# Kernel tuning notes

Measured on AMD Instinct MI355X. Metric: run time of the kernel, lower is better.

## Reference

```python
import jax, jax.numpy as jnp
import numpy as np
import math

NUM_HEADS = 16
THETA = 10000.0


def _rope(x, token_pos, theta):
    # x: [B, H, S, d_k]; token_pos: [S]
    d_k = x.shape[-1]
    freqs = 1.0 / theta ** (jnp.arange(0, d_k, 2, dtype=jnp.float32) / d_k)  # [d_k/2]
    angles = token_pos.astype(jnp.float32)[:, None] * freqs[None, :]         # [S, d_k/2]
    cos, sin = jnp.cos(angles), jnp.sin(angles)
    x1 = x[..., 0::2]
    x2 = x[..., 1::2]
    out1 = x1 * cos - x2 * sin
    out2 = x1 * sin + x2 * cos
    # interleave back: (..., d_k/2, 2) -> (..., d_k)
    return jnp.stack([out1, out2], axis=-1).reshape(x.shape)


def setup_inputs() -> dict:
    key = jax.random.key(0)
    ks = jax.random.split(key, 5)
    B, S, D = 4, 2048, 1024
    scale = 0.02
    return {
        "x": jax.random.normal(ks[0], (B, S, D), dtype=jnp.float32),
        "token_pos": jnp.arange(S, dtype=jnp.int64 if jax.config.jax_enable_x64 else jnp.int32),
        "Wq": jax.random.normal(ks[1], (D, D), dtype=jnp.float32) * scale,
        "Wk": jax.random.normal(ks[2], (D, D), dtype=jnp.float32) * scale,
        "Wv": jax.random.normal(ks[3], (D, D), dtype=jnp.float32) * scale,
        "Wo": jax.random.normal(ks[4], (D, D), dtype=jnp.float32) * scale,
    }


def reference(x, token_pos, Wq, Wk, Wv, Wo):
    B, S, D = x.shape
    H = NUM_HEADS
    d_k = D // H
    # projections (Linear without bias: y = x @ W^T, W is [out, in])
    def proj(W):
        y = jnp.einsum('bsd,ed->bse', x, W)
        return y.reshape(B, S, H, d_k).transpose(0, 2, 1, 3)  # [B,H,S,d_k]
    q, k, v = proj(Wq), proj(Wk), proj(Wv)
    q = _rope(q, token_pos, THETA)
    k = _rope(k, token_pos, THETA)
    scores = jnp.einsum('bhqd,bhkd->bhqk', q, k) / math.sqrt(d_k)
    causal = jnp.tril(jnp.ones((S, S), dtype=bool))
    scores = jnp.where(causal, scores, -jnp.inf)
    attn = jax.nn.softmax(scores, axis=-1)
    out = jnp.einsum('bhqk,bhkd->bhqd', attn, v)            # [B,H,S,d_k]
    out = out.transpose(0, 2, 1, 3).reshape(B, S, D)
    return jnp.einsum('bsd,ed->bse', out, Wo)
```

## Files before the change

### kernel.cpp

```cpp
#include <hip/hip_runtime.h>

typedef unsigned short u16;
typedef __bf16 bf16x8 __attribute__((ext_vector_type(8)));
typedef float f32x4 __attribute__((ext_vector_type(4)));
typedef u16 u16x8 __attribute__((ext_vector_type(8)));

#define B_ 4
#define S_ 2048
#define D_ 1024
#define H_ 16
#define LOG2E 1.44269504f

__device__ inline u16 f2bf(float f) {
  unsigned u = __float_as_uint(f);
  u = u + 0x7fffu + ((u >> 16) & 1u);
  return (u16)(u >> 16);
}
__device__ inline u16 f2bf_hw(float f) {
  __bf16 b = (__bf16)f;
  return __builtin_bit_cast(u16, b);
}
__device__ inline float bf2f(u16 h) {
  return __uint_as_float(((unsigned)h) << 16);
}
__device__ inline void gload_lds16(const u16* g, u16* l) {
  __builtin_amdgcn_global_load_lds((const __attribute__((address_space(1))) void*)g,
                                   (__attribute__((address_space(3))) void*)l, 16, 0, 0);
}
__device__ inline float fast_exp2(float x) {
  float r;
  asm("v_exp_f32 %0, %1" : "=v"(r) : "v"(x));
  return r;
}

__global__ __launch_bounds__(256) void k_f32_to_bf16(const float* __restrict__ src,
                                                     u16* __restrict__ dst, int n4) {
  int i = blockIdx.x * 256 + threadIdx.x;
  if (i >= n4) return;
  float4 v = reinterpret_cast<const float4*>(src)[i];
  ushort4 o;
  o.x = f2bf(v.x); o.y = f2bf(v.y); o.z = f2bf(v.z); o.w = f2bf(v.w);
  reinterpret_cast<ushort4*>(dst)[i] = o;
}

__global__ __launch_bounds__(256) void k_cvt_w4(const float* __restrict__ w0,
                                                const float* __restrict__ w1,
                                                const float* __restrict__ w2,
                                                const float* __restrict__ w3,
                                                u16* __restrict__ dst) {
  int i = blockIdx.x * 256 + threadIdx.x;
  const int tensor = i >> 18;
  const int local = i & 262143;
  const float* s = tensor == 0 ? w0 : tensor == 1 ? w1 : tensor == 2 ? w2 : w3;
  float4 v = reinterpret_cast<const float4*>(s)[local];
  ushort4 o;
  o.x = f2bf(v.x); o.y = f2bf(v.y); o.z = f2bf(v.z); o.w = f2bf(v.w);
  reinterpret_cast<ushort4*>(dst + (size_t)tensor * 1048576)[local] = o;
}

__global__ __launch_bounds__(256) void k_rope_table(const int* __restrict__ pos,
                                                    float2* __restrict__ tab) {
  int idx = blockIdx.x * 256 + threadIdx.x;
  if (idx >= S_ * 32) return;
  int s = idx >> 5, i = idx & 31;
  float freq = powf(10000.0f, -(float)i * (1.0f / 32.0f));
  float ang = (float)pos[s] * freq;
  float sn, c;
  sincosf(ang, &sn, &c);
  tab[idx] = make_float2(c, sn);
}

__global__ __launch_bounds__(256) void k_rope_k(u16* __restrict__ kb,
                                                const float2* __restrict__ tab) {
  int idx = blockIdx.x * 256 + threadIdx.x;
  const int row = idx >> 7;
  const int s = row & 2047;
  const int chunk = idx & 127;
  u16* p = kb + ((size_t)row << 10) + chunk * 8;
  u16x8 v = *reinterpret_cast<u16x8*>(p);
  const float4* tp = reinterpret_cast<const float4*>(tab + s * 32 + (chunk & 7) * 4);
  float4 t0 = tp[0], t1 = tp[1];
  float cc[4] = {t0.x, t0.z, t1.x, t1.z};
  float ss[4] = {t0.y, t0.w, t1.y, t1.w};
  u16x8 o;
#pragma unroll
  for (int u = 0; u < 4; u++) {
    float x1 = bf2f(v[2 * u]), x2 = bf2f(v[2 * u + 1]);
    o[2 * u]     = f2bf(x1 * cc[u] - x2 * ss[u]);
    o[2 * u + 1] = f2bf(x1 * ss[u] + x2 * cc[u]);
  }
  *reinterpret_cast<u16x8*>(p) = o;
}

__global__ __launch_bounds__(256) void k_gemm_qkv(const u16* __restrict__ A,
                                                  const u16* __restrict__ Bcat,
                                                  u16* __restrict__ Ccat,
                                                  u16* __restrict__ Vt) {
  __shared__ u16 As[128 * 64];
  __shared__ u16 Bs[128 * 64];
  const int K = 1024;
  const int swz = (blockIdx.x & 7) * 192 + (blockIdx.x >> 3);
  const int bx = swz % 24;
  const int by = swz / 24;
  const int m0 = by << 7, n0 = bx << 7;
  const int tid = threadIdx.x;
  const int lane = tid & 63;
  const int wv = tid >> 6;
  const int wm = (wv >> 1) << 6;
  const int wn = (wv & 1) << 6;
  const int r = lane & 15, g = lane >> 4;

  f32x4 acc[4][4] = {};

  const int srow0 = tid >> 3;
  const int scol = (((tid & 7) ^ ((tid >> 3) & 7)) * 8);
  const int csw = r & 7;

  for (int k0 = 0; k0 < K; k0 += 64) {
#pragma unroll
    for (int i = 0; i < 4; i++)
      gload_lds16(A + (size_t)(m0 + srow0 + 32 * i) * K + k0 + scol,
                  As + tid * 8 + i * 2048);
#pragma unroll
    for (int i = 0; i < 4; i++)
      gload_lds16(Bcat + (size_t)(n0 + srow0 + 32 * i) * K + k0 + scol,
                  Bs + tid * 8 + i * 2048);
    __syncthreads();
#pragma unroll
    for (int ks = 0; ks < 2; ks++) {
      bf16x8 af[4], bfr[4];
#pragma unroll
      for (int i = 0; i < 4; i++)
        af[i] = *reinterpret_cast<const bf16x8*>(
            &As[(wm + i * 16 + r) * 64 + (((ks * 4 + g) ^ csw) * 8)]);
#pragma unroll
      for (int t = 0; t < 4; t++)
        bfr[t] = *reinterpret_cast<const bf16x8*>(
            &Bs[(wn + t * 16 + r) * 64 + (((ks * 4 + g) ^ csw) * 8)]);
#pragma unroll
      for (int i = 0; i < 4; i++)
#pragma unroll
        for (int t = 0; t < 4; t++)
          acc[i][t] = __builtin_amdgcn_mfma_f32_16x16x32_bf16(af[i], bfr[t], acc[i][t], 0, 0, 0);
    }
    __syncthreads();
  }

  const int bq = n0 >> 10;
  const int c0 = n0 & 1023;
  if (bq == 2) {
#pragma unroll
    for (int i = 0; i < 4; i++) {
#pragma unroll
      for (int t = 0; t < 4; t++) {
        const int row = m0 + wm + i * 16 + g * 4;
        const int col = c0 + wn + t * 16 + r;
        const int b = row >> 11, s0 = row & 2047;
        const int h = col >> 6, d = col & 63;
        ushort4 o;
        o.x = f2bf(acc[i][t][0]); o.y = f2bf(acc[i][t][1]);
        o.z = f2bf(acc[i][t][2]); o.w = f2bf(acc[i][t][3]);
        *reinterpret_cast<ushort4*>(
            Vt + (((size_t)(b * 16 + h) * 64 + d) << 11) + s0) = o;
      }
    }
  } else {
    u16* Cb = Ccat + (size_t)bq * (8192 * 1024);
#pragma unroll
    for (int i = 0; i < 4; i++) {
#pragma unroll
      for (int t = 0; t < 4; t++) {
        const int row = m0 + wm + i * 16 + g * 4;
        const int col = c0 + wn + t * 16 + r;
#pragma unroll
        for (int j = 0; j < 4; j++)
          Cb[(size_t)(row + j) * 1024 + col] = f2bf(acc[i][t][j]);
      }
    }
  }
}

__global__ __launch_bounds__(256) void k_gemm_bt(const u16* __restrict__ A,
                                                 const u16* __restrict__ Bw,
                                                 float* __restrict__ C,
                                                 int M, int N, int K) {
  __shared__ u16 As[128 * 64];
  __shared__ u16 Bs[128 * 64];
  const int nbx = N >> 7;
  const int swz = (blockIdx.x & 7) * (gridDim.x >> 3) + (blockIdx.x >> 3);
  const int bx = swz % nbx;
  const int by = swz / nbx;
  const int m0 = by << 7, n0 = bx << 7;
  const int tid = threadIdx.x;
  const int lane = tid & 63;
  const int wv = tid >> 6;
  const int wm = (wv >> 1) << 6;
  const int wn = (wv & 1) << 6;
  const int r = lane & 15, g = lane >> 4;

  f32x4 acc[4][4] = {};

  const int srow0 = tid >> 3;
  const int scol = (((tid & 7) ^ ((tid >> 3) & 7)) * 8);
  const int csw = r & 7;

  for (int k0 = 0; k0 < K; k0 += 64) {
#pragma unroll
    for (int i = 0; i < 4; i++)
      gload_lds16(A + (size_t)(m0 + srow0 + 32 * i) * K + k0 + scol,
                  As + tid * 8 + i * 2048);
#pragma unroll
    for (int i = 0; i < 4; i++)
      gload_lds16(Bw + (size_t)(n0 + srow0 + 32 * i) * K + k0 + scol,
                  Bs + tid * 8 + i * 2048);
    __syncthreads();
#pragma unroll
    for (int ks = 0; ks < 2; ks++) {
      bf16x8 af[4], bfr[4];
#pragma unroll
      for (int i = 0; i < 4; i++)
        af[i] = *reinterpret_cast<const bf16x8*>(
            &As[(wm + i * 16 + r) * 64 + (((ks * 4 + g) ^ csw) * 8)]);
#pragma unroll
      for (int t = 0; t < 4; t++)
        bfr[t] = *reinterpret_cast<const bf16x8*>(
            &Bs[(wn + t * 16 + r) * 64 + (((ks * 4 + g) ^ csw) * 8)]);
#pragma unroll
      for (int i = 0; i < 4; i++)
#pragma unroll
        for (int t = 0; t < 4; t++)
          acc[i][t] = __builtin_amdgcn_mfma_f32_16x16x32_bf16(af[i], bfr[t], acc[i][t], 0, 0, 0);
    }
    __syncthreads();
  }

#pragma unroll
  for (int i = 0; i < 4; i++) {
#pragma unroll
    for (int t = 0; t < 4; t++) {
      const int row = m0 + wm + i * 16 + g * 4;
      const int col = n0 + wn + t * 16 + r;
#pragma unroll
      for (int j = 0; j < 4; j++)
        C[(size_t)(row + j) * N + col] = acc[i][t][j];
    }
  }
}

__global__ __launch_bounds__(256) void k_attn14(const u16* __restrict__ Q,
                                                const u16* __restrict__ Kb,
                                                const u16* __restrict__ Vt,
                                                const float2* __restrict__ tab,
                                                u16* __restrict__ O) {
  __shared__ u16 Ks[64 * 64];
  __shared__ u16 Vs[64 * 64];
  __shared__ u16 Ps[4][32 * 64];

  const int bh = (blockIdx.x & 7) * 8 + ((blockIdx.x >> 3) & 7);
  const int qt = 15 - (blockIdx.x >> 6);
  const int b = bh >> 4, h = bh & 15;
  const int tid = threadIdx.x;
  const int lane = tid & 63, w = tid >> 6;
  const int g = lane >> 4, r = lane & 15;

  const u16* Kbase = Kb + (size_t)(b * S_) * 1024 + h * 64;
  const u16* Vbase = Vt + (size_t)bh * 64 * 2048;

  const int srow = tid >> 3;
  const int scol = ((tid & 7) * 8) ^ ((srow & 7) * 8);
  const int rsw = (r & 7) * 8;

  const int qbase = qt << 7;
  const int qrow0 = qbase + (w << 5);

  const float QSC = 0.125f * LOG2E;
  bf16x8 qf[2][2];
#pragma unroll
  for (int f = 0; f < 2; f++) {
    const int s = qrow0 + f * 16 + r;
    const u16* qrow = Q + (size_t)(b * S_ + s) * 1024 + h * 64;
    qf[f][0] = *reinterpret_cast<const bf16x8*>(qrow + g * 8);
    qf[f][1] = *reinterpret_cast<const bf16x8*>(qrow + 32 + g * 8);
    const float4* tp = reinterpret_cast<const float4*>(tab + s * 32);
#pragma unroll
    for (int c = 0; c < 2; c++) {
      float4 t0 = tp[c * 8 + g * 2], t1 = tp[c * 8 + g * 2 + 1];
      float cc[4] = {t0.x, t0.z, t1.x, t1.z};
      float ss[4] = {t0.y, t0.w, t1.y, t1.w};
      bf16x8 q = qf[f][c];
#pragma unroll
      for (int u = 0; u < 4; u++) {
        float x1 = (float)q[2 * u], x2 = (float)q[2 * u + 1];
        q[2 * u]     = (__bf16)((x1 * cc[u] - x2 * ss[u]) * QSC);
        q[2 * u + 1] = (__bf16)((x1 * ss[u] + x2 * cc[u]) * QSC);
      }
      qf[f][c] = q;
    }
  }

  bf16x8 ones;
#pragma unroll
  for (int u = 0; u < 8; u++) ones[u] = (__bf16)1.0f;

  f32x4 o_acc[2][4] = {};
  f32x4 lacc[2] = {};
  u16* pb0 = &Ps[w][r * 64];
  u16* pb1 = &Ps[w][(16 + r) * 64];

  const u16* kp0 = Kbase + (size_t)srow * 1024 + scol;
  const u16* kp1 = kp0 + 32 * 1024;
  const u16* vp0 = Vbase + (size_t)srow * 2048 + scol;
  const u16* vp1 = vp0 + 32 * 2048;

  const int kend = qbase + 128;
  for (int k0 = 0; k0 < kend; k0 += 64) {
    gload_lds16(kp0, Ks + tid * 8);
    gload_lds16(kp1, Ks + tid * 8 + 2048);
    gload_lds16(vp0, Vs + tid * 8);
    gload_lds16(vp1, Vs + tid * 8 + 2048);
    kp0 += 64 * 1024; kp1 += 64 * 1024; vp0 += 64; vp1 += 64;
    __syncthreads();

    if (k0 <= qrow0 + 31) {
      const int rem0 = qrow0 + 15 - k0;
      const int rem1 = qrow0 + 31 - k0;
      const int ktlim0 = rem0 < 0 ? 0 : (rem0 >= 48 ? 4 : (rem0 >> 4) + 1);
      const int ktlim1 = rem1 >= 48 ? 4 : (rem1 >> 4) + 1;
      const bool mask0 = (k0 + 63 > qrow0);
      const bool mask1 = (k0 + 63 > qrow0 + 16);

#pragma unroll
      for (int kt = 0; kt < 4; kt++) {
        const int pc = (kt * 16 + g * 4) ^ rsw;
        if (kt >= ktlim1) {
          ushort4 z = {0, 0, 0, 0};
          *reinterpret_cast<ushort4*>(pb0 + pc) = z;
          *reinterpret_cast<ushort4*>(pb1 + pc) = z;
          continue;
        }
        const int krow = kt * 16 + r;
        bf16x8 kf0 = *reinterpret_cast<const bf16x8*>(&Ks[krow * 64 + ((g * 8) ^ rsw)]);
        bf16x8 kf1 = *reinterpret_cast<const bf16x8*>(&Ks[krow * 64 + ((32 + g * 8) ^ rsw)]);
        f32x4 s0 = {}, s1 = {};
        if (kt < ktlim0) {
          s0 = __builtin_amdgcn_mfma_f32_16x16x32_bf16(kf0, qf[0][0], s0, 0, 0, 0);
          s0 = __builtin_amdgcn_mfma_f32_16x16x32_bf16(kf1, qf[0][1], s0, 0, 0, 0);
        }
        s1 = __builtin_amdgcn_mfma_f32_16x16x32_bf16(kf0, qf[1][0], s1, 0, 0, 0);
        s1 = __builtin_amdgcn_mfma_f32_16x16x32_bf16(kf1, qf[1][1], s1, 0, 0, 0);

        const int colb = k0 + kt * 16 + g * 4;
        float p0[4], p1[4];
        if (kt < ktlim0) {
          if (mask0) {
#pragma unroll
            for (int j = 0; j < 4; j++)
              if (colb + j > qrow0 + r) s0[j] = -1e30f;
          }
#pragma unroll
          for (int j = 0; j < 4; j++) p0[j] = fast_exp2(s0[j]);
        } else {
#pragma unroll
          for (int j = 0; j < 4; j++) p0[j] = 0.f;
        }
        if (mask1) {
#pragma unroll
          for (int j = 0; j < 4; j++)
            if (colb + j > qrow0 + 16 + r) s1[j] = -1e30f;
        }
#pragma unroll
        for (int j = 0; j < 4; j++) p1[j] = fast_exp2(s1[j]);

        ushort4 w0, w1;
        w0.x = f2bf_hw(p0[0]); w0.y = f2bf_hw(p0[1]); w0.z = f2bf_hw(p0[2]); w0.w = f2bf_hw(p0[3]);
        w1.x = f2bf_hw(p1[0]); w1.y = f2bf_hw(p1[1]); w1.z = f2bf_hw(p1[2]); w1.w = f2bf_hw(p1[3]);
        *reinterpret_cast<ushort4*>(pb0 + pc) = w0;
        *reinterpret_cast<ushort4*>(pb1 + pc) = w1;
      }
      asm volatile("s_waitcnt lgkmcnt(0)" ::: "memory");

#pragma unroll
      for (int kc = 0; kc < 2; kc++) {
        const int cb = (kc * 32 + g * 8) ^ rsw;
        bf16x8 pf0 = *reinterpret_cast<const bf16x8*>(pb0 + cb);
        bf16x8 pf1 = *reinterpret_cast<const bf16x8*>(pb1 + cb);
        lacc[0] = __builtin_amdgcn_mfma_f32_16x16x32_bf16(pf0, ones, lacc[0], 0, 0, 0);
        lacc[1] = __builtin_amdgcn_mfma_f32_16x16x32_bf16(pf1, ones, lacc[1], 0, 0, 0);
#pragma unroll
        for (int dt = 0; dt < 4; dt++) {
          bf16x8 vf = *reinterpret_cast<const bf16x8*>(
              &Vs[(dt * 16 + r) * 64 + ((kc * 32 + g * 8) ^ rsw)]);
          o_acc[0][dt] = __builtin_amdgcn_mfma_f32_16x16x32_bf16(pf0, vf, o_acc[0][dt], 0, 0, 0);
          o_acc[1][dt] = __builtin_amdgcn_mfma_f32_16x16x32_bf16(pf1, vf, o_acc[1][dt], 0, 0, 0);
        }
      }
    }
    __syncthreads();
  }

#pragma unroll
  for (int f = 0; f < 2; f++) {
    u16* orow = O + (size_t)(b * S_ + qrow0 + f * 16) * 1024 + h * 64;
#pragma unroll
    for (int j = 0; j < 4; j++) {
      const float rln = 1.0f / lacc[f][j];
#pragma unroll
      for (int dt = 0; dt < 4; dt++)
        orow[(size_t)(g * 4 + j) * 1024 + dt * 16 + r] = f2bf(o_acc[f][dt][j] * rln);
    }
  }
}

extern "C" void kernel_launch(void* const* d_in, const int* in_sizes, int n_in,
                              void* d_out, int out_size, void* d_ws, size_t ws_size,
                              hipStream_t stream) {
  const float* x  = (const float*)d_in[0];
  const int*   pos = (const int*)d_in[1];
  const float* Wq = (const float*)d_in[2];
  const float* Wk = (const float*)d_in[3];
  const float* Wv = (const float*)d_in[4];
  const float* Wo = (const float*)d_in[5];
  float* out = (float*)d_out;

  char* ws = (char*)d_ws;
  size_t off = 0;
  auto alloc = [&](size_t bytes) {
    void* p = ws + off;
    off += (bytes + 255) & ~(size_t)255;
    return p;
  };
  const size_t XB = (size_t)8192 * 1024 * 2;
  u16* xb  = (u16*)alloc(XB);
  u16* wqb = (u16*)alloc((size_t)1024 * 1024 * 2);
  u16* wkb = (u16*)alloc((size_t)1024 * 1024 * 2);
  u16* wvb = (u16*)alloc((size_t)1024 * 1024 * 2);
  u16* wob = (u16*)alloc((size_t)1024 * 1024 * 2);
  u16* qb  = (u16*)alloc(XB);
  u16* kb  = (u16*)alloc(XB);
  u16* ob  = (u16*)alloc(XB);
  u16* vt  = (u16*)alloc(XB);
  float2* tab = (float2*)alloc((size_t)2048 * 32 * sizeof(float2));
  (void)wkb; (void)wvb;

  k_f32_to_bf16<<<8192, 256, 0, stream>>>(x, xb, 2097152);
  k_cvt_w4<<<4096, 256, 0, stream>>>(Wq, Wk, Wv, Wo, wqb);
  k_rope_table<<<256, 256, 0, stream>>>(pos, tab);

  k_gemm_qkv<<<1536, 256, 0, stream>>>(xb, wqb, qb, vt);

  k_rope_k<<<4096, 256, 0, stream>>>(kb, tab);

  k_attn14<<<1024, 256, 0, stream>>>(qb, kb, vt, tab, ob);

  k_gemm_bt<<<512, 256, 0, stream>>>(ob, wob, out, 8192, 1024, 1024);
}
```

Before: 183.0 us.

## Double-buffer LDS tiles in QKV and output projection GEMMs

Both projection GEMM kernels now keep two LDS buffers per operand and issue the global-to-LDS loads for the next K tile before computing on the current one. Explicit vmcnt waits and raw s_barrier calls replace the old load, sync, compute, sync sequence. The aim is to hide global-load latency behind the MFMA work. LDS use per block doubles to 64 KB, which may lower occupancy, and correctness now depends on the hand-set vmcnt counts.

```diff
diff --git a/kernel.cpp b/kernel.cpp
--- a/kernel.cpp
+++ b/kernel.cpp
@@ -96,8 +96,8 @@
                                                   const u16* __restrict__ Bcat,
                                                   u16* __restrict__ Ccat,
                                                   u16* __restrict__ Vt) {
-  __shared__ u16 As[128 * 64];
-  __shared__ u16 Bs[128 * 64];
+  __shared__ u16 As[2][128 * 64];
+  __shared__ u16 Bs[2][128 * 64];
   const int K = 1024;
   const int swz = (blockIdx.x & 7) * 192 + (blockIdx.x >> 3);
   const int bx = swz % 24;
@@ -116,35 +116,56 @@
   const int scol = (((tid & 7) ^ ((tid >> 3) & 7)) * 8);
   const int csw = r & 7;
 
-  for (int k0 = 0; k0 < K; k0 += 64) {
-#pragma unroll
-    for (int i = 0; i < 4; i++)
-      gload_lds16(A + (size_t)(m0 + srow0 + 32 * i) * K + k0 + scol,
-                  As + tid * 8 + i * 2048);
-#pragma unroll
-    for (int i = 0; i < 4; i++)
-      gload_lds16(Bcat + (size_t)(n0 + srow0 + 32 * i) * K + k0 + scol,
-                  Bs + tid * 8 + i * 2048);
-    __syncthreads();
+  const u16* Ab = A + (size_t)(m0 + srow0) * K + scol;
+  const u16* Bb = Bcat + (size_t)(n0 + srow0) * K + scol;
+
+#define STAGEQ(k0v, bf) do {                                       \
+    const u16* a_ = Ab + (k0v);                                    \
+    const u16* b_ = Bb + (k0v);                                    \
+    gload_lds16(a_,                &As[bf][0] + tid * 8);          \
+    gload_lds16(a_ + (size_t)32 * K, &As[bf][0] + tid * 8 + 2048); \
+    gload_lds16(a_ + (size_t)64 * K, &As[bf][0] + tid * 8 + 4096); \
+    gload_lds16(a_ + (size_t)96 * K, &As[bf][0] + tid * 8 + 6144); \
+    gload_lds16(b_,                &Bs[bf][0] + tid * 8);          \
+    gload_lds16(b_ + (size_t)32 * K, &Bs[bf][0] + tid * 8 + 2048); \
+    gload_lds16(b_ + (size_t)64 * K, &Bs[bf][0] + tid * 8 + 4096); \
+    gload_lds16(b_ + (size_t)96 * K, &Bs[bf][0] + tid * 8 + 6144); \
+  } while (0)
+
+  STAGEQ(0, 0);
+
+  for (int t = 0; t < 16; ++t) {
+    const int bsel = t & 1;
+    if (t < 15) {
+      STAGEQ((t + 1) * 64, bsel ^ 1);
+      asm volatile("s_waitcnt vmcnt(8)" ::: "memory");
+    } else {
+      asm volatile("s_waitcnt vmcnt(0)" ::: "memory");
+    }
+    __builtin_amdgcn_s_barrier();
+    asm volatile("" ::: "memory");
+
 #pragma unroll
     for (int ks = 0; ks < 2; ks++) {
       bf16x8 af[4], bfr[4];
 #pragma unroll
       for (int i = 0; i < 4; i++)
         af[i] = *reinterpret_cast<const bf16x8*>(
-            &As[(wm + i * 16 + r) * 64 + (((ks * 4 + g) ^ csw) * 8)]);
-#pragma unroll
-      for (int t = 0; t < 4; t++)
-        bfr[t] = *reinterpret_cast<const bf16x8*>(
-            &Bs[(wn + t * 16 + r) * 64 + (((ks * 4 + g) ^ csw) * 8)]);
+            &As[bsel][(wm + i * 16 + r) * 64 + (((ks * 4 + g) ^ csw) * 8)]);
+#pragma unroll
+      for (int t2 = 0; t2 < 4; t2++)
+        bfr[t2] = *reinterpret_cast<const bf16x8*>(
+            &Bs[bsel][(wn + t2 * 16 + r) * 64 + (((ks * 4 + g) ^ csw) * 8)]);
 #pragma unroll
       for (int i = 0; i < 4; i++)
 #pragma unroll
-        for (int t = 0; t < 4; t++)
-          acc[i][t] = __builtin_amdgcn_mfma_f32_16x16x32_bf16(af[i], bfr[t], acc[i][t], 0, 0, 0);
-    }
-    __syncthreads();
-  }
+        for (int t2 = 0; t2 < 4; t2++)
+          acc[i][t2] = __builtin_amdgcn_mfma_f32_16x16x32_bf16(af[i], bfr[t2], acc[i][t2], 0, 0, 0);
+    }
+    asm volatile("" ::: "memory");
+    __builtin_amdgcn_s_barrier();
+  }
+#undef STAGEQ
 
   const int bq = n0 >> 10;
   const int c0 = n0 & 1023;
@@ -184,8 +205,8 @@
                                                  const u16* __restrict__ Bw,
                                                  float* __restrict__ C,
                                                  int M, int N, int K) {
-  __shared__ u16 As[128 * 64];
-  __shared__ u16 Bs[128 * 64];
+  __shared__ u16 As[2][128 * 64];
+  __shared__ u16 Bs[2][128 * 64];
   const int nbx = N >> 7;
   const int swz = (blockIdx.x & 7) * (gridDim.x >> 3) + (blockIdx.x >> 3);
   const int bx = swz % nbx;
@@ -204,35 +225,57 @@
   const int scol = (((tid & 7) ^ ((tid >> 3) & 7)) * 8);
   const int csw = r & 7;
 
-  for (int k0 = 0; k0 < K; k0 += 64) {
-#pragma unroll
-    for (int i = 0; i < 4; i++)
-      gload_lds16(A + (size_t)(m0 + srow0 + 32 * i) * K + k0 + scol,
-                  As + tid * 8 + i * 2048);
-#pragma unroll
-    for (int i = 0; i < 4; i++)
-      gload_lds16(Bw + (size_t)(n0 + srow0 + 32 * i) * K + k0 + scol,
-                  Bs + tid * 8 + i * 2048);
-    __syncthreads();
+  const u16* Ab = A + (size_t)(m0 + srow0) * K + scol;
+  const u16* Bb = Bw + (size_t)(n0 + srow0) * K + scol;
+  const int nt = K >> 6;
+
+#define STAGEW(k0v, bf) do {                                       \
+    const u16* a_ = Ab + (k0v);                                    \
+    const u16* b_ = Bb + (k0v);                                    \
+    gload_lds16(a_,                &As[bf][0] + tid * 8);          \
+    gload_lds16(a_ + (size_t)32 * K, &As[bf][0] + tid * 8 + 2048); \
+    gload_lds16(a_ + (size_t)64 * K, &As[bf][0] + tid * 8 + 4096); \
+    gload_lds16(a_ + (size_t)96 * K, &As[bf][0] + tid * 8 + 6144); \
+    gload_lds16(b_,                &Bs[bf][0] + tid * 8);          \
+    gload_lds16(b_ + (size_t)32 * K, &Bs[bf][0] + tid * 8 + 2048); \
+    gload_lds16(b_ + (size_t)64 * K, &Bs[bf][0] + tid * 8 + 4096); \
+    gload_lds16(b_ + (size_t)96 * K, &Bs[bf][0] + tid * 8 + 6144); \
+  } while (0)
+
+  STAGEW(0, 0);
+
+  for (int t = 0; t < nt; ++t) {
+    const int bsel = t & 1;
+    if (t < nt - 1) {
+      STAGEW((t + 1) * 64, bsel ^ 1);
+      asm volatile("s_waitcnt vmcnt(8)" ::: "memory");
+    } else {
+      asm volatile("s_waitcnt vmcnt(0)" ::: "memory");
+    }
+    __builtin_amdgcn_s_barrier();
+    asm volatile("" ::: "memory");
+
 #pragma unroll
     for (int ks = 0; ks < 2; ks++) {
       bf16x8 af[4], bfr[4];
 #pragma unroll
       for (int i = 0; i < 4; i++)
         af[i] = *reinterpret_cast<const bf16x8*>(
-            &As[(wm + i * 16 + r) * 64 + (((ks * 4 + g) ^ csw) * 8)]);
-#pragma unroll
-      for (int t = 0; t < 4; t++)
-        bfr[t] = *reinterpret_cast<const bf16x8*>(
-            &Bs[(wn + t * 16 + r) * 64 + (((ks * 4 + g) ^ csw) * 8)]);
+            &As[bsel][(wm + i * 16 + r) * 64 + (((ks * 4 + g) ^ csw) * 8)]);
+#pragma unroll
+      for (int t2 = 0; t2 < 4; t2++)
+        bfr[t2] = *reinterpret_cast<const bf16x8*>(
+            &Bs[bsel][(wn + t2 * 16 + r) * 64 + (((ks * 4 + g) ^ csw) * 8)]);
 #pragma unroll
       for (int i = 0; i < 4; i++)
 #pragma unroll
-        for (int t = 0; t < 4; t++)
-          acc[i][t] = __builtin_amdgcn_mfma_f32_16x16x32_bf16(af[i], bfr[t], acc[i][t], 0, 0, 0);
-    }
-    __syncthreads();
-  }
+        for (int t2 = 0; t2 < 4; t2++)
+          acc[i][t2] = __builtin_amdgcn_mfma_f32_16x16x32_bf16(af[i], bfr[t2], acc[i][t2], 0, 0, 0);
+    }
+    asm volatile("" ::: "memory");
+    __builtin_amdgcn_s_barrier();
+  }
+#undef STAGEW
 
 #pragma unroll
   for (int i = 0; i < 4; i++) {
```

Result: no change. 180.2 us (-1.5%).
